# Kernel optimization log

Hardware: AMD Instinct MI355X
Metric: run time of the kernel (lower is better)

Reference implementation:

```python
import jax, jax.numpy as jnp
import numpy as np

HEADS = 4
DIM_HEAD = 64
MAP_SIZE = 16
SCALE = DIM_HEAD ** (-0.5)


def _split_heads(x):
    # torch rearrange 'b (dim_head heads) h w -> b heads (h w) dim_head'
    B, C, H, W = x.shape
    x = x.reshape(B, DIM_HEAD, HEADS, H * W)
    return jnp.transpose(x, (0, 2, 3, 1))  # [B, heads, N, dim_head]


def _merge_heads(x, H, W):
    # torch rearrange 'b heads (h w) dim_head -> b (dim_head heads) h w'
    B, h, N, d = x.shape
    return jnp.transpose(x, (0, 3, 1, 2)).reshape(B, d * h, H, W)


def setup_inputs() -> dict:
    key = jax.random.key(0)
    ks = jax.random.split(key, 6)
    feat = jax.random.normal(ks[0], (4, 256, 96, 96), jnp.float32)
    semantic_map = jax.random.normal(ks[1], (4, 256, 16, 16), jnp.float32)
    # 1x1 conv weights, shape [out_ch, in_ch]; scaled like fan-in init
    W_feat_qv = 0.05 * jax.random.normal(ks[2], (512, 256), jnp.float32)
    W_map_qv = 0.05 * jax.random.normal(ks[3], (512, 256), jnp.float32)
    W_feat_out = 0.05 * jax.random.normal(ks[4], (256, 256), jnp.float32)
    W_map_out = 0.05 * jax.random.normal(ks[5], (256, 256), jnp.float32)
    return {
        "feat": feat,
        "semantic_map": semantic_map,
        "W_feat_qv": W_feat_qv,
        "W_map_qv": W_map_qv,
        "W_feat_out": W_feat_out,
        "W_map_out": W_map_out,
    }


def reference(feat, semantic_map, W_feat_qv, W_map_qv, W_feat_out, W_map_out):
    B, C, H, W = feat.shape
    # 1x1 convs == per-pixel channel matmuls
    fqv = jnp.einsum("oc,bchw->bohw", W_feat_qv, feat)
    feat_q, feat_v = jnp.split(fqv, 2, axis=1)
    mqv = jnp.einsum("oc,bchw->bohw", W_map_qv, semantic_map)
    map_q, map_v = jnp.split(mqv, 2, axis=1)

    feat_q, feat_v = _split_heads(feat_q), _split_heads(feat_v)  # [B,h,N,d]
    map_q, map_v = _split_heads(map_q), _split_heads(map_v)      # [B,h,M,d]

    attn = jnp.einsum("bhid,bhjd->bhij", feat_q, map_q) * SCALE  # [B,h,N,M]
    feat_map_attn = jax.nn.softmax(attn, axis=-1)  # normalize over map tokens j
    map_feat_attn = jax.nn.softmax(attn, axis=-2)  # normalize over feat tokens i

    feat_o = jnp.einsum("bhij,bhjd->bhid", feat_map_attn, map_v)   # [B,h,N,d]
    map_o = jnp.einsum("bhji,bhjd->bhid", map_feat_attn, feat_v)   # [B,h,M,d]

    feat_o = _merge_heads(feat_o, H, W)
    map_o = _merge_heads(map_o, MAP_SIZE, MAP_SIZE)

    feat_out = jnp.einsum("oc,bchw->bohw", W_feat_out, feat_o)
    map_out = jnp.einsum("oc,bchw->bohw", W_map_out, map_o)
    return feat_out, map_out
```

## Files before the change

kernel.cpp:

```cpp
#include <hip/hip_runtime.h>
#include <stdint.h>

#define DI static __device__ __forceinline__

constexpr int NTOK = 9216;
constexpr float ATT_SCALE = 0.125f;

typedef short bf16x8 __attribute__((ext_vector_type(8)));
typedef float f32x4  __attribute__((ext_vector_type(4)));

DI f32x4 mfma16(bf16x8 a, bf16x8 b, f32x4 c) {
  return __builtin_amdgcn_mfma_f32_16x16x32_bf16(a, b, c, 0, 0, 0);
}

DI float lo2f(uint32_t u) { union { uint32_t i; float f; } v; v.i = u << 16; return v.f; }
DI float hi2f(uint32_t u) { union { uint32_t i; float f; } v; v.i = u & 0xffff0000u; return v.f; }
DI float b2f(uint16_t u) { union { uint32_t i; float f; } v; v.i = ((uint32_t)u) << 16; return v.f; }
DI uint16_t f2b(float f) {
  union { float f; uint32_t i; } v; v.f = f;
  uint32_t r = (v.i + 0x7fffu + ((v.i >> 16) & 1u)) >> 16;
  return (uint16_t)r;
}

template<int DT> DI float ld1(const void* p, size_t off) {
  if constexpr (DT) return b2f(((const uint16_t*)p)[off]);
  else              return ((const float*)p)[off];
}
template<int DT> DI void st1(void* p, size_t off, float v) {
  if constexpr (DT) ((uint16_t*)p)[off] = f2b(v);
  else              ((float*)p)[off] = v;
}

__global__ void detect_dtype(const uint32_t* __restrict__ w, int* __restrict__ flag) {
  const int l = threadIdx.x;
  int cl = 0;
  #pragma unroll
  for (int i = 0; i < 4; ++i) {
    const float b = b2f((uint16_t)(w[l + i * 64] & 0xffffu));
    const float ab = fabsf(b);
    cl += (ab > 1e-4f && ab < 0.5f) ? 1 : 0;
  }
  cl += __shfl_xor(cl, 1);  cl += __shfl_xor(cl, 2);  cl += __shfl_xor(cl, 4);
  cl += __shfl_xor(cl, 8);  cl += __shfl_xor(cl, 16); cl += __shfl_xor(cl, 32);
  if (l == 0) flag[0] = (cl >= 128) ? 1 : 0;
}

template<int DT>
DI void prep_w_body(const void* __restrict__ Wfqv, const void* __restrict__ Wfo,
                    uint16_t* __restrict__ WqvP, uint16_t* __restrict__ WfoP)
{
  const int r = blockIdx.x, c = threadIdx.x;
  if (r < 512) {
    const int sel = r >> 8, within = r & 255;
    const int h = within >> 6, d = within & 63;
    const int src = sel * 256 + d * 4 + h;
    WqvP[(size_t)r * 256 + c] = f2b(ld1<DT>(Wfqv, (size_t)src * 256 + c));
  } else {
    const int ro = r - 512;
    WfoP[(size_t)ro * 256 + c] =
        f2b(ld1<DT>(Wfo, (size_t)ro * 256 + (c & 63) * 4 + (c >> 6)));
  }
}
__global__ __launch_bounds__(256) void prep_w(
    const void* Wfqv, const void* Wfo, uint16_t* WqvP, uint16_t* WfoP,
    const int* __restrict__ flag)
{
  if (flag[0]) prep_w_body<1>(Wfqv, Wfo, WqvP, WfoP);
  else         prep_w_body<0>(Wfqv, Wfo, WqvP, WfoP);
}

constexpr int P0 = 280;

template<int DT>
DI void gemm0_body(uint16_t* Xs, const uint16_t* __restrict__ WqvP,
                   const void* __restrict__ X,
                   uint16_t* __restrict__ FQ, uint16_t* __restrict__ FVt)
{
  const int tid = threadIdx.x;
  const int w = tid >> 6, lane = tid & 63;
  const int l = lane & 15, quad = lane >> 4;
  const int n0 = blockIdx.x * 64;
  const int bb = blockIdx.y;
  const size_t bh = (size_t)bb * 4 + w;

  {
    const int nh = (tid & 1) * 32;
    #pragma unroll
    for (int p = 0; p < 2; ++p) {
      const int c = p * 128 + (tid >> 1);
      const size_t g = ((size_t)bb * 256 + c) * NTOK + n0 + nh;
      if constexpr (DT) {
        #pragma unroll
        for (int u = 0; u < 4; ++u) {
          const uint4 v = *(const uint4*)((const uint16_t*)X + g + u * 8);
          const uint16_t* pk = (const uint16_t*)&v;
          #pragma unroll
          for (int j = 0; j < 8; ++j)
            Xs[(size_t)(nh + u * 8 + j) * P0 + c] = pk[j];
        }
      } else {
        #pragma unroll
        for (int u = 0; u < 8; ++u) {
          const float4 v = *(const float4*)((const float*)X + g + u * 4);
          Xs[(size_t)(nh + u * 4 + 0) * P0 + c] = f2b(v.x);
          Xs[(size_t)(nh + u * 4 + 1) * P0 + c] = f2b(v.y);
          Xs[(size_t)(nh + u * 4 + 2) * P0 + c] = f2b(v.z);
          Xs[(size_t)(nh + u * 4 + 3) * P0 + c] = f2b(v.w);
        }
      }
    }
  }
  __syncthreads();

  f32x4 acc[8][4];
  #pragma unroll
  for (int a = 0; a < 8; ++a)
    #pragma unroll
    for (int b = 0; b < 4; ++b) { acc[a][b].x = 0.f; acc[a][b].y = 0.f; acc[a][b].z = 0.f; acc[a][b].w = 0.f; }

  for (int ks = 0; ks < 8; ++ks) {
    bf16x8 af[8];
    #pragma unroll
    for (int mt = 0; mt < 8; ++mt) {
      const int arow = (mt >> 2) * 256 + w * 64 + (mt & 3) * 16 + l;
      af[mt] = *(const bf16x8*)(WqvP + (size_t)arow * 256 + ks * 32 + quad * 8);
    }
    #pragma unroll
    for (int nt = 0; nt < 4; ++nt) {
      const bf16x8 bv = *(const bf16x8*)(Xs + (size_t)(nt * 16 + l) * P0 + ks * 32 + quad * 8);
      #pragma unroll
      for (int mt = 0; mt < 8; ++mt)
        acc[mt][nt] = mfma16(af[mt], bv, acc[mt][nt]);
    }
  }
  #pragma unroll
  for (int mt = 0; mt < 8; ++mt)
    #pragma unroll
    for (int nt = 0; nt < 4; ++nt) {
      const int n = n0 + nt * 16 + l;
      if (mt < 4) {
        union { uint16_t h[4]; uint2 u; } pk;
        #pragma unroll
        for (int r = 0; r < 4; ++r) pk.h[r] = f2b(acc[mt][nt][r]);
        *(uint2*)(FQ + (bh * NTOK + n) * 64 + mt * 16 + quad * 4) = pk.u;
      } else {
        const int itile = n >> 5, io = n & 31;
        #pragma unroll
        for (int r = 0; r < 4; ++r)
          FVt[(((size_t)bh * 288 + itile) * 64 + (mt - 4) * 16 + quad * 4 + r) * 32 + io] =
              f2b(acc[mt][nt][r]);
      }
    }
}
__global__ __launch_bounds__(256) void gemm0_mfma(
    const uint16_t* WqvP, const void* X, uint16_t* FQ, uint16_t* FVt,
    const int* __restrict__ flag)
{
  __shared__ __align__(16) uint16_t Xs[64 * P0];
  if (flag[0]) gemm0_body<1>(Xs, WqvP, X, FQ, FVt);
  else         gemm0_body<0>(Xs, WqvP, X, FQ, FVt);
}

template<int DT>
DI void gemm1_body(const uint16_t* __restrict__ WfoP, const uint16_t* __restrict__ FO,
                   void* __restrict__ out)
{
  const int tid = threadIdx.x;
  const int w = tid >> 6, lane = tid & 63;
  const int l = lane & 15, quad = lane >> 4;
  const int n0 = blockIdx.x * 256;
  const int o0 = blockIdx.y * 64;
  const int bb = blockIdx.z;

  f32x4 acc[4][4];
  #pragma unroll
  for (int a = 0; a < 4; ++a)
    #pragma unroll
    for (int b = 0; b < 4; ++b) { acc[a][b].x = 0.f; acc[a][b].y = 0.f; acc[a][b].z = 0.f; acc[a][b].w = 0.f; }

  for (int ks = 0; ks < 8; ++ks) {
    const int h2 = ks >> 1;
    const int doff = (ks & 1) * 32 + quad * 8;
    bf16x8 af[4];
    #pragma unroll
    for (int mt = 0; mt < 4; ++mt)
      af[mt] = *(const bf16x8*)(WfoP + (size_t)(o0 + mt * 16 + l) * 256 + ks * 32 + quad * 8);
    #pragma unroll
    for (int nt = 0; nt < 4; ++nt) {
      const int n = n0 + w * 64 + nt * 16 + l;
      const bf16x8 bv = *(const bf16x8*)(FO + ((size_t)(bb * 4 + h2) * NTOK + n) * 64 + doff);
      #pragma unroll
      for (int mt = 0; mt < 4; ++mt)
        acc[mt][nt] = mfma16(af[mt], bv, acc[mt][nt]);
    }
  }
  #pragma unroll
  for (int mt = 0; mt < 4; ++mt)
    #pragma unroll
    for (int nt = 0; nt < 4; ++nt) {
      const int n = n0 + w * 64 + nt * 16 + l;
      #pragma unroll
      for (int r = 0; r < 4; ++r)
        st1<DT>(out, ((size_t)bb * 256 + o0 + mt * 16 + quad * 4 + r) * NTOK + n,
                acc[mt][nt][r]);
    }
}
__global__ __launch_bounds__(256) void gemm1_mfma(
    const uint16_t* WfoP, const uint16_t* FO, void* out,
    const int* __restrict__ flag)
{
  if (flag[0]) gemm1_body<1>(WfoP, FO, out);
  else         gemm1_body<0>(WfoP, FO, out);
}

template<int DT>
DI void map_qv_body(const void* __restrict__ Wqv, const void* __restrict__ smap,
                    uint16_t* __restrict__ MQ, uint16_t* __restrict__ MVT)
{
  const int o = blockIdx.x, bb = blockIdx.y, m = threadIdx.x;
  float acc = 0.f;
  #pragma unroll 8
  for (int c = 0; c < 256; ++c)
    acc += ld1<DT>(Wqv, (size_t)o * 256 + c) *
           ld1<DT>(smap, (size_t)bb * 65536 + (size_t)c * 256 + m);
  const int oc = o & 255;
  const int h = oc & 3, d = oc >> 2;
  if (o < 256) MQ[(((size_t)bb * 4 + h) * 256 + m) * 64 + d] = f2b(acc);
  else         MVT[(((size_t)bb * 4 + h) * 64 + d) * 256 + m] = f2b(acc);
}
__global__ __launch_bounds__(256) void map_qv(
    const void* Wqv, const void* smap, uint16_t* MQ, uint16_t* MVT,
    const int* __restrict__ flag)
{
  if (flag[0]) map_qv_body<1>(Wqv, smap, MQ, MVT);
  else         map_qv_body<0>(Wqv, smap, MQ, MVT);
}

constexpr int PJ = 280;
constexpr int PI = 40;
constexpr int PO = 72;
constexpr int NGRP = 36;

__global__ __launch_bounds__(256, 3) void attn_mfma(
    const uint16_t* __restrict__ FQ, const uint16_t* __restrict__ FVt,
    const uint16_t* __restrict__ MQ, const uint16_t* __restrict__ MVT,
    uint16_t* __restrict__ FO, uint16_t* __restrict__ P)
{
  __shared__ __align__(16) uint16_t Esh[32 * PJ];
  __shared__ __align__(16) uint16_t ETsh[256 * PI];
  __shared__ __align__(16) uint16_t Osh[32 * PO];
  __shared__ float RS[4][32];
  const int tid = threadIdx.x;
  const int w = tid >> 6;
  const int lane = tid & 63;
  const int l = lane & 15, quad = lane >> 4;
  const int blk = blockIdx.x, bh = blockIdx.y;
  const uint16_t* FQh  = FQ  + (size_t)bh * NTOK * 64;
  const uint16_t* FVth = FVt + (size_t)bh * 288 * 64 * 32;
  const uint16_t* MQh  = MQ  + (size_t)bh * 256 * 64;
  const uint16_t* MVTh = MVT + (size_t)bh * 64 * 256;
  uint16_t* FOh = FO + (size_t)bh * NTOK * 64;

  bf16x8 kb[4][2];
  #pragma unroll
  for (int jt = 0; jt < 4; ++jt) {
    const int j = w * 64 + jt * 16 + l;
    kb[jt][0] = *(const bf16x8*)(MQh + (size_t)j * 64 + quad * 8);
    kb[jt][1] = *(const bf16x8*)(MQh + (size_t)j * 64 + 32 + quad * 8);
  }
  bf16x8 avr[8];
  #pragma unroll
  for (int ks = 0; ks < 8; ++ks)
    avr[ks] = *(const bf16x8*)(MVTh + (size_t)(w * 16 + l) * 256 + ks * 32 + quad * 8);

  f32x4 numacc[4][4];
  #pragma unroll
  for (int a = 0; a < 4; ++a)
    #pragma unroll
    for (int b = 0; b < 4; ++b) { numacc[a][b].x = 0.f; numacc[a][b].y = 0.f; numacc[a][b].z = 0.f; numacc[a][b].w = 0.f; }
  float csum[4] = {0.f, 0.f, 0.f, 0.f};

  for (int t = 0; t < 8; ++t) {
    const int it = blk * 8 + t;
    const int i0 = it * 32;

    bf16x8 qa[2][2];
    #pragma unroll
    for (int mt = 0; mt < 2; ++mt)
      #pragma unroll
      for (int kbi = 0; kbi < 2; ++kbi)
        qa[mt][kbi] = *(const bf16x8*)(FQh + (size_t)(i0 + mt * 16 + l) * 64 + kbi * 32 + quad * 8);

    float rsum[2][4] = {{0.f,0.f,0.f,0.f},{0.f,0.f,0.f,0.f}};
    #pragma unroll
    for (int jt = 0; jt < 4; ++jt) {
      const int j0 = w * 64 + jt * 16;
      #pragma unroll
      for (int mt = 0; mt < 2; ++mt) {
        f32x4 acc = {0.f, 0.f, 0.f, 0.f};
        acc = mfma16(qa[mt][0], kb[jt][0], acc);
        acc = mfma16(qa[mt][1], kb[jt][1], acc);
        union { uint16_t h[4]; uint2 u; } pk;
        #pragma unroll
        for (int r = 0; r < 4; ++r) {
          const float e = __expf(acc[r] * ATT_SCALE);
          rsum[mt][r] += e;
          csum[jt] += e;
          pk.h[r] = f2b(e);
          Esh[(mt * 16 + quad * 4 + r) * PJ + j0 + l] = pk.h[r];
        }
        *(uint2*)(ETsh + (size_t)(j0 + l) * PI + mt * 16 + quad * 4) = pk.u;
      }
    }
    #pragma unroll
    for (int mt = 0; mt < 2; ++mt)
      #pragma unroll
      for (int r = 0; r < 4; ++r) {
        float v = rsum[mt][r];
        v += __shfl_xor(v, 1); v += __shfl_xor(v, 2);
        v += __shfl_xor(v, 4); v += __shfl_xor(v, 8);
        if (l == 0) RS[w][mt * 16 + quad * 4 + r] = v;
      }
    __syncthreads();

    bf16x8 av[4];
    #pragma unroll
    for (int mt = 0; mt < 4; ++mt)
      av[mt] = *(const bf16x8*)(FVth + ((size_t)it * 64 + mt * 16 + l) * 32 + quad * 8);

    {
      float rinv[2];
      #pragma unroll
      for (int nt = 0; nt < 2; ++nt) {
        const int i_ = nt * 16 + l;
        rinv[nt] = 1.f / (RS[0][i_] + RS[1][i_] + RS[2][i_] + RS[3][i_]);
      }
      f32x4 oacc[2];
      oacc[0].x=0.f;oacc[0].y=0.f;oacc[0].z=0.f;oacc[0].w=0.f;
      oacc[1]=oacc[0];
      #pragma unroll
      for (int ks = 0; ks < 8; ++ks) {
        #pragma unroll
        for (int nt = 0; nt < 2; ++nt) {
          const bf16x8 bv = *(const bf16x8*)(Esh + (size_t)(nt * 16 + l) * PJ + ks * 32 + quad * 8);
          oacc[nt] = mfma16(avr[ks], bv, oacc[nt]);
        }
      }
      #pragma unroll
      for (int nt = 0; nt < 2; ++nt) {
        union { uint16_t h[4]; uint2 u; } pk;
        #pragma unroll
        for (int r = 0; r < 4; ++r) pk.h[r] = f2b(oacc[nt][r] * rinv[nt]);
        *(uint2*)(Osh + (nt * 16 + l) * PO + w * 16 + quad * 4) = pk.u;
      }
    }

    #pragma unroll
    for (int mt = 0; mt < 4; ++mt) {
      #pragma unroll
      for (int nt2 = 0; nt2 < 4; ++nt2) {
        const bf16x8 bv = *(const bf16x8*)(ETsh + (size_t)(w * 64 + nt2 * 16 + l) * PI + quad * 8);
        numacc[mt][nt2] = mfma16(av[mt], bv, numacc[mt][nt2]);
      }
    }
    __syncthreads();

    {
      const int ti = tid >> 3, c = tid & 7;
      *(uint4*)(FOh + (size_t)(i0 + ti) * 64 + c * 8) =
          *(const uint4*)(Osh + ti * PO + c * 8);
    }
  }

  uint16_t* Pb = P + ((size_t)bh * NGRP + blk) * 65 * 256;
  #pragma unroll
  for (int mt = 0; mt < 4; ++mt)
    #pragma unroll
    for (int nt2 = 0; nt2 < 4; ++nt2)
      #pragma unroll
      for (int r = 0; r < 4; ++r)
        Pb[(mt * 16 + quad * 4 + r) * 256 + w * 64 + nt2 * 16 + l] =
            f2b(numacc[mt][nt2][r]);
  #pragma unroll
  for (int jt = 0; jt < 4; ++jt) {
    float v = csum[jt];
    v += __shfl_xor(v, 16); v += __shfl_xor(v, 32);
    if (quad == 0) Pb[64 * 256 + w * 64 + jt * 16 + l] = f2b(v);
  }
}

__global__ __launch_bounds__(256) void reduce_map(
    const uint16_t* __restrict__ P, uint16_t* __restrict__ MO)
{
  const int idx = blockIdx.x * 256 + threadIdx.x;
  const int bh = idx >> 14;
  const int d = (idx >> 8) & 63;
  const int j = idx & 255;
  const size_t base = (size_t)bh * NGRP * 65 * 256;
  float num = 0.f, cs = 0.f;
  #pragma unroll 6
  for (int g = 0; g < NGRP; ++g) {
    num += b2f(P[base + ((size_t)g * 65 + d) * 256 + j]);
    cs  += b2f(P[base + ((size_t)g * 65 + 64) * 256 + j]);
  }
  const float v = num / cs;
  const int b = bh >> 2, h = bh & 3;
  MO[((size_t)b * 256 + (d * 4 + h)) * 256 + j] = f2b(v);
}

template<int DT>
DI void map_out_body(const void* __restrict__ Wmo, const uint16_t* __restrict__ MO,
                     void* __restrict__ out)
{
  const int o = blockIdx.x, bb = blockIdx.y, m = threadIdx.x;
  float acc = 0.f;
  #pragma unroll 8
  for (int c = 0; c < 256; ++c)
    acc += ld1<DT>(Wmo, (size_t)o * 256 + c) *
           b2f(MO[((size_t)bb * 256 + c) * 256 + m]);
  const size_t MAP_OFS = (size_t)4 * 256 * NTOK;
  st1<DT>(out, MAP_OFS + ((size_t)bb * 256 + o) * 256 + m, acc);
}
__global__ __launch_bounds__(256) void map_out_k(
    const void* Wmo, const uint16_t* MO, void* out, const int* __restrict__ flag)
{
  if (flag[0]) map_out_body<1>(Wmo, MO, out);
  else         map_out_body<0>(Wmo, MO, out);
}

extern "C" void kernel_launch(void* const* d_in, const int* in_sizes, int n_in,
                              void* d_out, int out_size, void* d_ws, size_t ws_size,
                              hipStream_t stream) {
  (void)in_sizes; (void)n_in; (void)out_size; (void)ws_size;
  const void* feat = d_in[0];
  const void* smap = d_in[1];
  const void* Wfqv = d_in[2];
  const void* Wmqv = d_in[3];
  const void* Wfo  = d_in[4];
  const void* Wmo  = d_in[5];
  char* ws = (char*)d_ws;

  const size_t BIG = (size_t)16 * 64 * NTOK * 2;
  const size_t SML = (size_t)16 * 256 * 64 * 2;
  const size_t FQ_OFF  = 0;
  const size_t FVT_OFF = FQ_OFF + BIG;
  const size_t MQ_OFF  = FVT_OFF + BIG;
  const size_t MVT_OFF = MQ_OFF + SML;
  const size_t MO_OFF  = MVT_OFF + SML;
  const size_t WQP_OFF = MO_OFF + (size_t)4 * 256 * 256 * 2;
  const size_t WFP_OFF = WQP_OFF + (size_t)512 * 256 * 2;
  const size_t FLAG_OFF = WFP_OFF + (size_t)256 * 256 * 2;

  uint16_t* FQ   = (uint16_t*)(ws + FQ_OFF);
  uint16_t* FVt  = (uint16_t*)(ws + FVT_OFF);
  uint16_t* MQ   = (uint16_t*)(ws + MQ_OFF);
  uint16_t* MVT  = (uint16_t*)(ws + MVT_OFF);
  uint16_t* MO   = (uint16_t*)(ws + MO_OFF);
  uint16_t* WqvP = (uint16_t*)(ws + WQP_OFF);
  uint16_t* WfoP = (uint16_t*)(ws + WFP_OFF);
  int* FLAG   = (int*)(ws + FLAG_OFF);

  uint16_t* P = (uint16_t*)d_out;

  detect_dtype<<<dim3(1), dim3(64), 0, stream>>>((const uint32_t*)Wfqv, FLAG);
  prep_w<<<dim3(768), 256, 0, stream>>>(Wfqv, Wfo, WqvP, WfoP, FLAG);
  gemm0_mfma<<<dim3(144, 4), 256, 0, stream>>>(WqvP, feat, FQ, FVt, FLAG);
  map_qv<<<dim3(512, 4), 256, 0, stream>>>(Wmqv, smap, MQ, MVT, FLAG);
  attn_mfma<<<dim3(NGRP, 16), 256, 0, stream>>>(FQ, FVt, MQ, MVT, FQ, P);
  reduce_map<<<dim3(1024), 256, 0, stream>>>(P, MO);
  gemm1_mfma<<<dim3(36, 4, 4), 256, 0, stream>>>(WfoP, FQ, d_out, FLAG);
  map_out_k<<<dim3(256, 4), 256, 0, stream>>>(Wmo, MO, d_out, FLAG);
}
```

Baseline: 290.1 us.

## Replace transposed-exp LDS buffer with cross-lane shuffles and raise occupancy

The transposed exp tile (ETsh) is no longer staged in shared memory. Each wave rebuilds the MFMA B operand for the map-side accumulation from its own packed exp values using __shfl, which cuts LDS use and round-trips. The MQ and MVT operand fragments are now reloaded from global memory inside the loop instead of being held in registers for the whole kernel, and launch bounds are raised from 3 to 4 blocks per SM. This trades extra shuffles and repeated global/L2 loads for lower LDS and register pressure and higher occupancy.

```diff
diff --git a/kernel.cpp b/kernel.cpp
--- a/kernel.cpp
+++ b/kernel.cpp
@@ -237,17 +237,15 @@
 }
 
 constexpr int PJ = 280;
-constexpr int PI = 40;
 constexpr int PO = 72;
 constexpr int NGRP = 36;
 
-__global__ __launch_bounds__(256, 3) void attn_mfma(
+__global__ __launch_bounds__(256, 4) void attn_mfma(
     const uint16_t* __restrict__ FQ, const uint16_t* __restrict__ FVt,
     const uint16_t* __restrict__ MQ, const uint16_t* __restrict__ MVT,
     uint16_t* __restrict__ FO, uint16_t* __restrict__ P)
 {
   __shared__ __align__(16) uint16_t Esh[32 * PJ];
-  __shared__ __align__(16) uint16_t ETsh[256 * PI];
   __shared__ __align__(16) uint16_t Osh[32 * PO];
   __shared__ float RS[4][32];
   const int tid = threadIdx.x;
@@ -261,24 +259,15 @@
   const uint16_t* MVTh = MVT + (size_t)bh * 64 * 256;
   uint16_t* FOh = FO + (size_t)bh * NTOK * 64;
 
-  bf16x8 kb[4][2];
-  #pragma unroll
-  for (int jt = 0; jt < 4; ++jt) {
-    const int j = w * 64 + jt * 16 + l;
-    kb[jt][0] = *(const bf16x8*)(MQh + (size_t)j * 64 + quad * 8);
-    kb[jt][1] = *(const bf16x8*)(MQh + (size_t)j * 64 + 32 + quad * 8);
-  }
-  bf16x8 avr[8];
-  #pragma unroll
-  for (int ks = 0; ks < 8; ++ks)
-    avr[ks] = *(const bf16x8*)(MVTh + (size_t)(w * 16 + l) * 256 + ks * 32 + quad * 8);
-
   f32x4 numacc[4][4];
   #pragma unroll
   for (int a = 0; a < 4; ++a)
     #pragma unroll
     for (int b = 0; b < 4; ++b) { numacc[a][b].x = 0.f; numacc[a][b].y = 0.f; numacc[a][b].z = 0.f; numacc[a][b].w = 0.f; }
   float csum[4] = {0.f, 0.f, 0.f, 0.f};
+
+  const int srcA = l + ((quad & 1) << 5);
+  const int srcB = srcA + 16;
 
   for (int t = 0; t < 8; ++t) {
     const int it = blk * 8 + t;
@@ -291,15 +280,18 @@
       for (int kbi = 0; kbi < 2; ++kbi)
         qa[mt][kbi] = *(const bf16x8*)(FQh + (size_t)(i0 + mt * 16 + l) * 64 + kbi * 32 + quad * 8);
 
+    uint2 pku[4][2];
     float rsum[2][4] = {{0.f,0.f,0.f,0.f},{0.f,0.f,0.f,0.f}};
     #pragma unroll
     for (int jt = 0; jt < 4; ++jt) {
       const int j0 = w * 64 + jt * 16;
+      const bf16x8 kb0 = *(const bf16x8*)(MQh + (size_t)(j0 + l) * 64 + quad * 8);
+      const bf16x8 kb1 = *(const bf16x8*)(MQh + (size_t)(j0 + l) * 64 + 32 + quad * 8);
       #pragma unroll
       for (int mt = 0; mt < 2; ++mt) {
         f32x4 acc = {0.f, 0.f, 0.f, 0.f};
-        acc = mfma16(qa[mt][0], kb[jt][0], acc);
-        acc = mfma16(qa[mt][1], kb[jt][1], acc);
+        acc = mfma16(qa[mt][0], kb0, acc);
+        acc = mfma16(qa[mt][1], kb1, acc);
         union { uint16_t h[4]; uint2 u; } pk;
         #pragma unroll
         for (int r = 0; r < 4; ++r) {
@@ -309,9 +301,15 @@
           pk.h[r] = f2b(e);
           Esh[(mt * 16 + quad * 4 + r) * PJ + j0 + l] = pk.h[r];
         }
-        *(uint2*)(ETsh + (size_t)(j0 + l) * PI + mt * 16 + quad * 4) = pk.u;
-      }
-    }
+        pku[jt][mt] = pk.u;
+      }
+    }
+
+    bf16x8 av[4];
+    #pragma unroll
+    for (int mt = 0; mt < 4; ++mt)
+      av[mt] = *(const bf16x8*)(FVth + ((size_t)it * 64 + mt * 16 + l) * 32 + quad * 8);
+
     #pragma unroll
     for (int mt = 0; mt < 2; ++mt)
       #pragma unroll
@@ -321,12 +319,28 @@
         v += __shfl_xor(v, 4); v += __shfl_xor(v, 8);
         if (l == 0) RS[w][mt * 16 + quad * 4 + r] = v;
       }
+
+    #pragma unroll
+    for (int nt2 = 0; nt2 < 4; ++nt2) {
+      const int a0 = __shfl((int)pku[nt2][0].x, srcA);
+      const int a1 = __shfl((int)pku[nt2][0].y, srcA);
+      const int a2 = __shfl((int)pku[nt2][0].x, srcB);
+      const int a3 = __shfl((int)pku[nt2][0].y, srcB);
+      const int b0 = __shfl((int)pku[nt2][1].x, srcA);
+      const int b1 = __shfl((int)pku[nt2][1].y, srcA);
+      const int b2 = __shfl((int)pku[nt2][1].x, srcB);
+      const int b3 = __shfl((int)pku[nt2][1].y, srcB);
+      const bool hi = (quad >> 1) != 0;
+      union { int i[4]; bf16x8 v; } bu;
+      bu.i[0] = hi ? b0 : a0;
+      bu.i[1] = hi ? b1 : a1;
+      bu.i[2] = hi ? b2 : a2;
+      bu.i[3] = hi ? b3 : a3;
+      #pragma unroll
+      for (int mt = 0; mt < 4; ++mt)
+        numacc[mt][nt2] = mfma16(av[mt], bu.v, numacc[mt][nt2]);
+    }
     __syncthreads();
-
-    bf16x8 av[4];
-    #pragma unroll
-    for (int mt = 0; mt < 4; ++mt)
-      av[mt] = *(const bf16x8*)(FVth + ((size_t)it * 64 + mt * 16 + l) * 32 + quad * 8);
 
     {
       float rinv[2];
@@ -340,10 +354,11 @@
       oacc[1]=oacc[0];
       #pragma unroll
       for (int ks = 0; ks < 8; ++ks) {
+        const bf16x8 avr = *(const bf16x8*)(MVTh + (size_t)(w * 16 + l) * 256 + ks * 32 + quad * 8);
         #pragma unroll
         for (int nt = 0; nt < 2; ++nt) {
           const bf16x8 bv = *(const bf16x8*)(Esh + (size_t)(nt * 16 + l) * PJ + ks * 32 + quad * 8);
-          oacc[nt] = mfma16(avr[ks], bv, oacc[nt]);
+          oacc[nt] = mfma16(avr, bv, oacc[nt]);
         }
       }
       #pragma unroll
@@ -352,15 +367,6 @@
         #pragma unroll
         for (int r = 0; r < 4; ++r) pk.h[r] = f2b(oacc[nt][r] * rinv[nt]);
         *(uint2*)(Osh + (nt * 16 + l) * PO + w * 16 + quad * 4) = pk.u;
-      }
-    }
-
-    #pragma unroll
-    for (int mt = 0; mt < 4; ++mt) {
-      #pragma unroll
-      for (int nt2 = 0; nt2 < 4; ++nt2) {
-        const bf16x8 bv = *(const bf16x8*)(ETsh + (size_t)(w * 64 + nt2 * 16 + l) * PI + quad * 8);
-        numacc[mt][nt2] = mfma16(av[mt], bv, numacc[mt][nt2]);
       }
     }
     __syncthreads();
```

Result: slower. 347.2 us (+19.7%).
